# Kernel tuning notes

Measured on AMD Instinct MI355X. Metric: run time of the kernel, lower is better.

## Reference

```python
import jax, jax.numpy as jnp
import numpy as np

B, S, CIN, H, W = 4, 16, 32, 64, 64
HID = 64


def conv2d(x, w, b=None):
    # x: (N,C,H,W), w: (O,I,kh,kw), stride 1, padding 1 (SAME for k=3)
    y = jax.lax.conv_general_dilated(
        x, w, window_strides=(1, 1), padding=[(1, 1), (1, 1)],
        dimension_numbers=("NCHW", "OIHW", "NCHW"))
    if b is not None:
        y = y + b[None, :, None, None]
    return y


def log_g(x):
    # log of g(x) = x+0.5 if x>=0 else sigmoid(x); safe double-where for grads
    pos = jnp.where(x >= 0, x, 0.0)
    return jnp.where(x >= 0, jnp.log(pos + 0.5), -jax.nn.softplus(-x))


def mingru_gate_hidden(gate, hidden, h_prev):
    # gate, hidden: (B,S,C,H,W); h_prev: (B,1,C,H,W), positive
    log_z = -jax.nn.softplus(-gate)        # log sigmoid(gate)
    log_coeffs = -jax.nn.softplus(gate)    # log (1 - sigmoid(gate))
    log_h0 = jnp.log(h_prev)
    log_values = jnp.concatenate([log_h0, log_z + log_g(hidden)], axis=1)  # (B,S+1,...)
    a_star = jnp.pad(jnp.cumsum(log_coeffs, axis=1),
                     ((0, 0), (1, 0), (0, 0), (0, 0), (0, 0)))             # (B,S+1,...)
    log_h = a_star + jax.lax.cumlogsumexp(log_values - a_star, axis=1)
    return jnp.exp(log_h)[:, 1:]  # (B,S,C,H,W)


def _layer(inp, Wg, bg, Rw):
    b_, s_ = inp.shape[:2]
    flat = inp.reshape(b_ * s_, *inp.shape[2:])
    y = conv2d(flat, Wg, bg)
    y = y.reshape(b_, s_, y.shape[1], y.shape[2], y.shape[3])
    gate, hidden = jnp.split(y, 2, axis=2)
    # init_hidden_state: g(zeros) == 0.5 everywhere
    h0 = jnp.full((b_, 1) + gate.shape[2:], 0.5, dtype=inp.dtype)
    out = mingru_gate_hidden(gate, hidden, h0)
    h_next = out[:, -1:]
    if Rw is not None:
        res = conv2d(flat, Rw).reshape(b_, s_, -1, out.shape[3], out.shape[4])
    else:
        res = inp  # res_align is Identity
    return out + res, h_next


def setup_inputs() -> dict:
    key = jax.random.key(0)
    ks = jax.random.split(key, 4)
    x = jax.random.normal(ks[0], (B, S, CIN, H, W), jnp.float32)
    s0 = 1.0 / np.sqrt(CIN * 9)
    s1 = 1.0 / np.sqrt(HID * 9)
    W0 = jax.random.normal(ks[1], (2 * HID, CIN, 3, 3), jnp.float32) * s0
    b0 = jnp.zeros((2 * HID,), jnp.float32)
    R0 = jax.random.normal(ks[2], (HID, CIN, 3, 3), jnp.float32) * s0  # res align 32->64
    W1 = jax.random.normal(ks[3], (2 * HID, HID, 3, 3), jnp.float32) * s1
    b1 = jnp.zeros((2 * HID,), jnp.float32)
    return {"x": x, "W0": W0, "b0": b0, "R0": R0, "W1": W1, "b1": b1}


def reference(x, W0, b0, R0, W1, b1):
    out, h0 = _layer(x, W0, b0, R0)
    out, h1 = _layer(out, W1, b1, None)
    return out, h0, h1
```

## Files before the change

kernel.cpp:

```cpp
#include <hip/hip_runtime.h>

typedef short short8  __attribute__((ext_vector_type(8)));
typedef short shortx4 __attribute__((ext_vector_type(4)));
typedef float floatx4 __attribute__((ext_vector_type(4)));
typedef unsigned short u16;

static __device__ __forceinline__ float bits2f(u16 s) {
    return __builtin_bit_cast(float, (unsigned)s << 16);
}
static __device__ __forceinline__ u16 f2bits(float f) {
    return __builtin_bit_cast(u16, (__bf16)f);
}

#define SS 16

__global__ void prep_kernel(const float* W0, const float* R0, const float* W1,
                            u16* wt0f, u16* wt1) {
    const int i = blockIdx.x * 256 + threadIdx.x;
    if (i < 55296) {
        const int t = i / 6144, r = i % 6144, ko = r >> 5, ci = r & 31;
        wt0f[i] = f2bits(ko < 128 ? W0[(ko * 32 + ci) * 9 + t]
                                  : R0[((ko - 128) * 32 + ci) * 9 + t]);
    } else if (i < 55296 + 73728) {
        const int j = i - 55296;
        const int t = j / 8192, r = j % 8192, ko = r >> 6, ci = r & 63;
        wt1[j] = f2bits(W1[(ko * 64 + ci) * 9 + t]);
    }
}

__global__ void transpose_kernel(const float* __restrict__ x, u16* __restrict__ xT) {
    const int img = blockIdx.x >> 6, h = blockIdx.x & 63;
    const int gq = threadIdx.x & 3, w = threadIdx.x >> 2;
    short8 o;
#pragma unroll
    for (int k = 0; k < 8; ++k)
        o[k] = (short)f2bits(x[((size_t)img * 32 + gq * 8 + k) * 4096 + h * 64 + w]);
    ((short8*)xT)[((size_t)(img * 64 + h) * 64 + w) * 4 + gq] = o;
}

__global__ __launch_bounds__(256, 2)
void fused_layer0_kernel(const u16* __restrict__ X, const u16* __restrict__ wt,
                         const float* __restrict__ bias,
                         u16* __restrict__ x1out, float* __restrict__ hlast) {
    __shared__ short8 lds[4 * 18 * 4];

    const int tid = threadIdx.x;
    const int l   = tid & 63;
    const int wv  = tid >> 6;
    const int c16 = l & 15;
    const int q16 = l >> 4;

    const int bid = blockIdx.x;
    const int b   = bid >> 7;
    const int h0  = ((bid >> 2) & 31) * 2;
    const int w0  = (bid & 3) * 16;

    const short8* wtv = (const short8*)wt;
    short8 af[9][3];
#pragma unroll
    for (int t = 0; t < 9; ++t)
#pragma unroll
        for (int g = 0; g < 3; ++g)
            af[t][g] = wtv[(size_t)(t * 192 + (wv + g * 4) * 16 + c16) * 4 + q16];

    const floatx4 biasg = *(const floatx4*)(bias + wv * 16 + q16 * 4);
    const floatx4 biash = *(const floatx4*)(bias + 64 + wv * 16 + q16 * 4);

    int ldsoff[2], goff[2];
    bool gval[2];
#pragma unroll
    for (int k = 0; k < 2; ++k) {
        const int idx = tid + k * 256;
        const int row = (idx >= 216) ? 3 : (idx >= 144) ? 2 : (idx >= 72) ? 1 : 0;
        const int rem = idx - row * 72;
        const int colrel = rem >> 2, q = rem & 3;
        const int hh = h0 - 1 + row;
        const int gc = w0 - 1 + colrel;
        ldsoff[k] = (row * 18 + colrel) * 4 + ((q + colrel) & 3);
        gval[k]   = (idx < 288) && ((unsigned)hh < 64u) && ((unsigned)gc < 64u);
        goff[k]   = (hh * 64 + gc) * 4 + q;
    }
    const bool k1 = (tid < 32);

    float hs[2][4];
#pragma unroll
    for (int m = 0; m < 2; ++m)
#pragma unroll
        for (int r = 0; r < 4; ++r) hs[m][r] = 0.5f;

    const short8* Xg = (const short8*)X;
    const short8 z8 = {0, 0, 0, 0, 0, 0, 0, 0};
    shortx4* x1v = (shortx4*)x1out;

    short8 v0, v1;
    {
        const short8* base = Xg + (size_t)(b * 16) * 16384;
        v0 = gval[0] ? base[goff[0]] : z8;
        v1 = gval[1] ? base[goff[1]] : z8;
    }

    for (int s = 0; s < SS; ++s) {
        lds[ldsoff[0]] = v0;
        if (k1) lds[ldsoff[1]] = v1;
        __syncthreads();

        if (s + 1 < SS) {
            const short8* base = Xg + (size_t)(b * 16 + s + 1) * 16384;
            v0 = gval[0] ? base[goff[0]] : z8;
            v1 = gval[1] ? base[goff[1]] : z8;
        }

        floatx4 acc[3][2];
#pragma unroll
        for (int m = 0; m < 2; ++m) {
            acc[0][m] = biasg; acc[1][m] = biash;
            acc[2][m] = floatx4{0.0f, 0.0f, 0.0f, 0.0f};
        }
#pragma unroll
        for (int t = 0; t < 9; ++t) {
            const int dy = t / 3, dx = t - dy * 3;
#pragma unroll
            for (int m = 0; m < 2; ++m) {
                const int row = m + dy;
                const int lc  = c16 + dx;
                const short8 bf = lds[(row * 18 + lc) * 4 + ((q16 + lc) & 3)];
#pragma unroll
                for (int g = 0; g < 3; ++g)
                    acc[g][m] = __builtin_amdgcn_mfma_f32_16x16x32_bf16(
                        af[t][g], bf, acc[g][m], 0, 0, 0);
            }
        }

#pragma unroll
        for (int m = 0; m < 2; ++m) {
            shortx4 ov;
#pragma unroll
            for (int r = 0; r < 4; ++r) {
                const float g   = acc[0][m][r];
                const float hid = acc[1][m][r];
                const float zz  = 1.0f / (1.0f + __expf(-g));
                const float gg  = (hid >= 0.0f) ? (hid + 0.5f)
                                                : (1.0f / (1.0f + __expf(-hid)));
                hs[m][r] = hs[m][r] + zz * (gg - hs[m][r]);
                ov[r] = (short)f2bits(hs[m][r] + acc[2][m][r]);
            }
            const size_t px = ((size_t)(b * 16 + s) * 64 + (h0 + m)) * 64
                              + w0 + c16;
            x1v[px * 16 + wv * 4 + q16] = ov;
        }
        __syncthreads();
    }

    float* hp = hlast + ((size_t)(b * 64) + (wv * 16 + q16 * 4)) * 4096
                      + h0 * 64 + w0 + c16;
#pragma unroll
    for (int m = 0; m < 2; ++m)
#pragma unroll
        for (int r = 0; r < 4; ++r)
            hp[(size_t)r * 4096 + m * 64] = hs[m][r];
}

__global__ __launch_bounds__(256, 2)
void fused_layer1_kernel(const u16* __restrict__ X, const u16* __restrict__ wt,
                         const float* __restrict__ bias,
                         float* __restrict__ out, float* __restrict__ hlast) {
    __shared__ short8 lds[4 * 18 * 8];

    const int tid = threadIdx.x;
    const int l   = tid & 63;
    const int wv  = tid >> 6;
    const int c16 = l & 15;
    const int q16 = l >> 4;

    const int bid = blockIdx.x;
    const int b   = bid >> 7;
    const int h0  = ((bid >> 2) & 31) * 2;
    const int w0  = (bid & 3) * 16;

    const short8* wtv = (const short8*)wt;
    short8 af[2][9][2];
#pragma unroll
    for (int ch = 0; ch < 2; ++ch)
#pragma unroll
        for (int t = 0; t < 9; ++t)
#pragma unroll
            for (int g = 0; g < 2; ++g)
                af[ch][t][g] =
                    wtv[(size_t)(t * 128 + (wv + g * 4) * 16 + c16) * 8 + ch * 4 + q16];

    const floatx4 biasg = *(const floatx4*)(bias + wv * 16 + q16 * 4);
    const floatx4 biash = *(const floatx4*)(bias + 64 + wv * 16 + q16 * 4);

    int ldsoff[3], goff[3];
    bool gval[3];
#pragma unroll
    for (int k = 0; k < 3; ++k) {
        const int idx = tid + k * 256;
        const int row = (idx >= 432) ? 3 : (idx >= 288) ? 2 : (idx >= 144) ? 1 : 0;
        const int rem = idx - row * 144;
        const int colrel = rem >> 3, q = rem & 7;
        const int hh = h0 - 1 + row;
        const int gc = w0 - 1 + colrel;
        ldsoff[k] = (row * 18 + colrel) * 8 + ((q + colrel) & 7);
        gval[k]   = (idx < 576) && ((unsigned)hh < 64u) && ((unsigned)gc < 64u);
        goff[k]   = (hh * 64 + gc) * 8 + q;
    }
    const bool k2 = (tid < 64);

    float hs[2][4];
#pragma unroll
    for (int m = 0; m < 2; ++m)
#pragma unroll
        for (int r = 0; r < 4; ++r) hs[m][r] = 0.5f;

    float* op = out + ((size_t)(b * 16) * 64 + (wv * 16 + q16 * 4)) * 4096
                    + h0 * 64 + w0 + c16;

    const short8* Xg = (const short8*)X;
    const short8 z8 = {0, 0, 0, 0, 0, 0, 0, 0};

    short8 v0, v1, v2;
    {
        const short8* base = Xg + (size_t)(b * 16) * 32768;
        v0 = gval[0] ? base[goff[0]] : z8;
        v1 = gval[1] ? base[goff[1]] : z8;
        v2 = gval[2] ? base[goff[2]] : z8;
    }

    for (int s = 0; s < SS; ++s) {
        lds[ldsoff[0]] = v0;
        lds[ldsoff[1]] = v1;
        if (k2) lds[ldsoff[2]] = v2;
        __syncthreads();

        if (s + 1 < SS) {
            const short8* base = Xg + (size_t)(b * 16 + s + 1) * 32768;
            v0 = gval[0] ? base[goff[0]] : z8;
            v1 = gval[1] ? base[goff[1]] : z8;
            v2 = gval[2] ? base[goff[2]] : z8;
        }

        floatx4 acc[2][2];
#pragma unroll
        for (int m = 0; m < 2; ++m) { acc[0][m] = biasg; acc[1][m] = biash; }
#pragma unroll
        for (int ch = 0; ch < 2; ++ch)
#pragma unroll
            for (int t = 0; t < 9; ++t) {
                const int dy = t / 3, dx = t - dy * 3;
#pragma unroll
                for (int m = 0; m < 2; ++m) {
                    const int row = m + dy;
                    const int lc  = c16 + dx;
                    const short8 bf =
                        lds[(row * 18 + lc) * 8 + ((ch * 4 + q16 + lc) & 7)];
                    acc[0][m] = __builtin_amdgcn_mfma_f32_16x16x32_bf16(
                        af[ch][t][0], bf, acc[0][m], 0, 0, 0);
                    acc[1][m] = __builtin_amdgcn_mfma_f32_16x16x32_bf16(
                        af[ch][t][1], bf, acc[1][m], 0, 0, 0);
                }
            }

        float* ops = op + (size_t)s * 262144;
        const int qres = wv * 2 + (q16 >> 1);
#pragma unroll
        for (int m = 0; m < 2; ++m) {
            const int rowc = 1 + m;
            const int lcc  = 1 + c16;
            const shortx4 rr = *(const shortx4*)(
                (const short*)&lds[(rowc * 18 + lcc) * 8 + ((qres + lcc) & 7)]
                + (q16 & 1) * 4);
#pragma unroll
            for (int r = 0; r < 4; ++r) {
                const float g   = acc[0][m][r];
                const float hid = acc[1][m][r];
                const float zz  = 1.0f / (1.0f + __expf(-g));
                const float gg  = (hid >= 0.0f) ? (hid + 0.5f)
                                                : (1.0f / (1.0f + __expf(-hid)));
                hs[m][r] = hs[m][r] + zz * (gg - hs[m][r]);
                const float o = hs[m][r] + bits2f((u16)rr[r]);
                ops[(size_t)r * 4096 + m * 64] = o;
            }
        }
        __syncthreads();
    }

    float* hp = hlast + ((size_t)(b * 64) + (wv * 16 + q16 * 4)) * 4096
                      + h0 * 64 + w0 + c16;
#pragma unroll
    for (int m = 0; m < 2; ++m)
#pragma unroll
        for (int r = 0; r < 4; ++r)
            hp[(size_t)r * 4096 + m * 64] = hs[m][r];
}

extern "C" void kernel_launch(void* const* d_in, const int* in_sizes, int n_in,
                              void* d_out, int out_size, void* d_ws, size_t ws_size,
                              hipStream_t stream) {
    const float* x  = (const float*)d_in[0];
    const float* W0 = (const float*)d_in[1];
    const float* b0 = (const float*)d_in[2];
    const float* R0 = (const float*)d_in[3];
    const float* W1 = (const float*)d_in[4];
    const float* b1 = (const float*)d_in[5];

    float* out = (float*)d_out;
    float* h0o = out + (size_t)16777216;
    float* h1o = h0o + (size_t)1048576;

    char* ws = (char*)d_ws;
    u16*   wt0f = (u16*)ws;
    u16*   wt1  = (u16*)(ws + 110592);
    u16*   xT   = (u16*)(ws + (size_t)(1  << 20));
    u16*   x1   = (u16*)(ws + (size_t)(18 << 20));

    prep_kernel<<<504, 256, 0, stream>>>(W0, R0, W1, wt0f, wt1);
    transpose_kernel<<<4096, 256, 0, stream>>>(x, xT);

    fused_layer0_kernel<<<512, 256, 0, stream>>>(xT, wt0f, b0, x1, h0o);

    fused_layer1_kernel<<<512, 256, 0, stream>>>(x1, wt1, b1, out, h1o);
}
```

Before: 183.1 us.

## Double-buffer LDS tiles across timesteps and merge prep with transpose kernel

Both fused layer kernels now keep two LDS buffers and prefetch global data two steps ahead, so the next tile is written to LDS while the current one is consumed. This aims to remove one barrier per timestep and hide global-load latency behind the MFMA work. The weight prep and input transpose kernels are merged into a single launch to save one kernel launch. In exchange, LDS use and register pressure grow, and the fully unrolled 16-step loop makes the code larger. With only one barrier left per step, correctness depends on that barrier also protecting the buffer that is overwritten next.

```diff
diff --git a/kernel.cpp b/kernel.cpp
--- a/kernel.cpp
+++ b/kernel.cpp
@@ -14,9 +14,21 @@
 
 #define SS 16
 
-__global__ void prep_kernel(const float* W0, const float* R0, const float* W1,
-                            u16* wt0f, u16* wt1) {
-    const int i = blockIdx.x * 256 + threadIdx.x;
+__global__ void prep_transpose_kernel(const float* __restrict__ x, u16* __restrict__ xT,
+                                      const float* W0, const float* R0, const float* W1,
+                                      u16* wt0f, u16* wt1) {
+    const int bid = blockIdx.x;
+    if (bid < 4096) {
+        const int img = bid >> 6, h = bid & 63;
+        const int gq = threadIdx.x & 3, w = threadIdx.x >> 2;
+        short8 o;
+#pragma unroll
+        for (int k = 0; k < 8; ++k)
+            o[k] = (short)f2bits(x[((size_t)img * 32 + gq * 8 + k) * 4096 + h * 64 + w]);
+        ((short8*)xT)[((size_t)(img * 64 + h) * 64 + w) * 4 + gq] = o;
+        return;
+    }
+    const int i = (bid - 4096) * 256 + threadIdx.x;
     if (i < 55296) {
         const int t = i / 6144, r = i % 6144, ko = r >> 5, ci = r & 31;
         wt0f[i] = f2bits(ko < 128 ? W0[(ko * 32 + ci) * 9 + t]
@@ -28,21 +40,11 @@
     }
 }
 
-__global__ void transpose_kernel(const float* __restrict__ x, u16* __restrict__ xT) {
-    const int img = blockIdx.x >> 6, h = blockIdx.x & 63;
-    const int gq = threadIdx.x & 3, w = threadIdx.x >> 2;
-    short8 o;
-#pragma unroll
-    for (int k = 0; k < 8; ++k)
-        o[k] = (short)f2bits(x[((size_t)img * 32 + gq * 8 + k) * 4096 + h * 64 + w]);
-    ((short8*)xT)[((size_t)(img * 64 + h) * 64 + w) * 4 + gq] = o;
-}
-
 __global__ __launch_bounds__(256, 2)
 void fused_layer0_kernel(const u16* __restrict__ X, const u16* __restrict__ wt,
                          const float* __restrict__ bias,
                          u16* __restrict__ x1out, float* __restrict__ hlast) {
-    __shared__ short8 lds[4 * 18 * 4];
+    __shared__ short8 lds[2][4 * 18 * 4];
 
     const int tid = threadIdx.x;
     const int l   = tid & 63;
@@ -92,22 +94,33 @@
     const short8 z8 = {0, 0, 0, 0, 0, 0, 0, 0};
     shortx4* x1v = (shortx4*)x1out;
 
-    short8 v0, v1;
+    short8 vW0, vW1;
     {
         const short8* base = Xg + (size_t)(b * 16) * 16384;
-        v0 = gval[0] ? base[goff[0]] : z8;
-        v1 = gval[1] ? base[goff[1]] : z8;
-    }
-
+        vW0 = gval[0] ? base[goff[0]] : z8;
+        vW1 = gval[1] ? base[goff[1]] : z8;
+    }
+    lds[0][ldsoff[0]] = vW0;
+    if (k1) lds[0][ldsoff[1]] = vW1;
+    {
+        const short8* base = Xg + (size_t)(b * 16 + 1) * 16384;
+        vW0 = gval[0] ? base[goff[0]] : z8;
+        vW1 = gval[1] ? base[goff[1]] : z8;
+    }
+    __syncthreads();
+
+#pragma unroll
     for (int s = 0; s < SS; ++s) {
-        lds[ldsoff[0]] = v0;
-        if (k1) lds[ldsoff[1]] = v1;
-        __syncthreads();
+        const int cur = s & 1;
 
         if (s + 1 < SS) {
-            const short8* base = Xg + (size_t)(b * 16 + s + 1) * 16384;
-            v0 = gval[0] ? base[goff[0]] : z8;
-            v1 = gval[1] ? base[goff[1]] : z8;
+            lds[cur ^ 1][ldsoff[0]] = vW0;
+            if (k1) lds[cur ^ 1][ldsoff[1]] = vW1;
+        }
+        if (s + 2 < SS) {
+            const short8* base = Xg + (size_t)(b * 16 + s + 2) * 16384;
+            vW0 = gval[0] ? base[goff[0]] : z8;
+            vW1 = gval[1] ? base[goff[1]] : z8;
         }
 
         floatx4 acc[3][2];
@@ -123,7 +136,7 @@
             for (int m = 0; m < 2; ++m) {
                 const int row = m + dy;
                 const int lc  = c16 + dx;
-                const short8 bf = lds[(row * 18 + lc) * 4 + ((q16 + lc) & 3)];
+                const short8 bf = lds[cur][(row * 18 + lc) * 4 + ((q16 + lc) & 3)];
 #pragma unroll
                 for (int g = 0; g < 3; ++g)
                     acc[g][m] = __builtin_amdgcn_mfma_f32_16x16x32_bf16(
@@ -164,7 +177,7 @@
 void fused_layer1_kernel(const u16* __restrict__ X, const u16* __restrict__ wt,
                          const float* __restrict__ bias,
                          float* __restrict__ out, float* __restrict__ hlast) {
-    __shared__ short8 lds[4 * 18 * 8];
+    __shared__ short8 lds[2][4 * 18 * 8];
 
     const int tid = threadIdx.x;
     const int l   = tid & 63;
@@ -219,25 +232,38 @@
     const short8* Xg = (const short8*)X;
     const short8 z8 = {0, 0, 0, 0, 0, 0, 0, 0};
 
-    short8 v0, v1, v2;
+    short8 vW0, vW1, vW2;
     {
         const short8* base = Xg + (size_t)(b * 16) * 32768;
-        v0 = gval[0] ? base[goff[0]] : z8;
-        v1 = gval[1] ? base[goff[1]] : z8;
-        v2 = gval[2] ? base[goff[2]] : z8;
-    }
-
+        vW0 = gval[0] ? base[goff[0]] : z8;
+        vW1 = gval[1] ? base[goff[1]] : z8;
+        vW2 = gval[2] ? base[goff[2]] : z8;
+    }
+    lds[0][ldsoff[0]] = vW0;
+    lds[0][ldsoff[1]] = vW1;
+    if (k2) lds[0][ldsoff[2]] = vW2;
+    {
+        const short8* base = Xg + (size_t)(b * 16 + 1) * 32768;
+        vW0 = gval[0] ? base[goff[0]] : z8;
+        vW1 = gval[1] ? base[goff[1]] : z8;
+        vW2 = gval[2] ? base[goff[2]] : z8;
+    }
+    __syncthreads();
+
+#pragma unroll
     for (int s = 0; s < SS; ++s) {
-        lds[ldsoff[0]] = v0;
-        lds[ldsoff[1]] = v1;
-        if (k2) lds[ldsoff[2]] = v2;
-        __syncthreads();
+        const int cur = s & 1;
 
         if (s + 1 < SS) {
-            const short8* base = Xg + (size_t)(b * 16 + s + 1) * 32768;
-            v0 = gval[0] ? base[goff[0]] : z8;
-            v1 = gval[1] ? base[goff[1]] : z8;
-            v2 = gval[2] ? base[goff[2]] : z8;
+            lds[cur ^ 1][ldsoff[0]] = vW0;
+            lds[cur ^ 1][ldsoff[1]] = vW1;
+            if (k2) lds[cur ^ 1][ldsoff[2]] = vW2;
+        }
+        if (s + 2 < SS) {
+            const short8* base = Xg + (size_t)(b * 16 + s + 2) * 32768;
+            vW0 = gval[0] ? base[goff[0]] : z8;
+            vW1 = gval[1] ? base[goff[1]] : z8;
+            vW2 = gval[2] ? base[goff[2]] : z8;
         }
 
         floatx4 acc[2][2];
@@ -253,7 +279,7 @@
                     const int row = m + dy;
                     const int lc  = c16 + dx;
                     const short8 bf =
-                        lds[(row * 18 + lc) * 8 + ((ch * 4 + q16 + lc) & 7)];
+                        lds[cur][(row * 18 + lc) * 8 + ((ch * 4 + q16 + lc) & 7)];
                     acc[0][m] = __builtin_amdgcn_mfma_f32_16x16x32_bf16(
                         af[ch][t][0], bf, acc[0][m], 0, 0, 0);
                     acc[1][m] = __builtin_amdgcn_mfma_f32_16x16x32_bf16(
@@ -268,7 +294,7 @@
             const int rowc = 1 + m;
             const int lcc  = 1 + c16;
             const shortx4 rr = *(const shortx4*)(
-                (const short*)&lds[(rowc * 18 + lcc) * 8 + ((qres + lcc) & 7)]
+                (const short*)&lds[cur][(rowc * 18 + lcc) * 8 + ((qres + lcc) & 7)]
                 + (q16 & 1) * 4);
 #pragma unroll
             for (int r = 0; r < 4; ++r) {
@@ -314,8 +340,7 @@
     u16*   xT   = (u16*)(ws + (size_t)(1  << 20));
     u16*   x1   = (u16*)(ws + (size_t)(18 << 20));
 
-    prep_kernel<<<504, 256, 0, stream>>>(W0, R0, W1, wt0f, wt1);
-    transpose_kernel<<<4096, 256, 0, stream>>>(x, xT);
+    prep_transpose_kernel<<<4600, 256, 0, stream>>>(x, xT, W0, R0, W1, wt0f, wt1);
 
     fused_layer0_kernel<<<512, 256, 0, stream>>>(xT, wt0f, b0, x1, h0o);
 
```

New measurement: 191.3 us. 1.05x slower.
